# Kernel tuning notes

Measured on AMD Instinct MI355X. Metric: run time of the kernel, lower is better.

## Reference

```python
import jax, jax.numpy as jnp
from jax import lax
import numpy as np

ALPHA = 0.5   # init alpha
TEMP = 0.1    # init temp (used in nt_xent_loss)
TEMP2 = 0.05  # hardcoded temperature inside nt_xent_loss2
EPS = 1e-12

N, D, C = 4096, 128, 20


def setup_inputs() -> dict:
    key = jax.random.key(0)
    k1, k2, k3 = jax.random.split(key, 3)
    cls_feats = jax.random.normal(k1, (N, D), dtype=jnp.float32)
    predicts = jax.random.normal(k2, (N, C), dtype=jnp.float32)
    targets = jax.random.randint(k3, (N,), 0, C)
    return {"cls_feats": cls_feats, "predicts": predicts, "targets": targets}


def _forward(cls_feats, predicts, targets):
    n = cls_feats.shape[0]
    # F.normalize(dim=-1): x / max(||x||, eps)
    norms = jnp.maximum(jnp.linalg.norm(cls_feats, axis=-1, keepdims=True), EPS)
    feats = cls_feats / norms

    # --- cross entropy (mean reduction) ---
    logp_cls = jax.nn.log_softmax(predicts, axis=-1)
    ce_loss = -jnp.mean(jnp.take_along_axis(logp_cls, targets[:, None], axis=1))

    same = (targets[:, None] == targets[None, :]).astype(feats.dtype)  # [N,N]
    diff = 1.0 - same

    # --- nt_xent_loss (supervised contrastive, mask excludes diagonal) ---
    mask = same * (1.0 - jnp.eye(n, dtype=feats.dtype))
    logits = jnp.matmul(feats, feats.T) / TEMP
    logits = logits - lax.stop_gradient(jnp.max(logits, axis=1, keepdims=True))
    exp_logits = jnp.exp(logits) * mask
    log_prob = logits - jnp.log(jnp.sum(exp_logits, axis=1, keepdims=True) + EPS)
    mask_sum = jnp.sum(mask, axis=1)
    mask_sum = jnp.where(mask_sum == 0, 1.0, mask_sum)
    cl_loss = -jnp.mean(jnp.sum(mask * log_prob, axis=1) / mask_sum)

    # --- nt_xent_loss2, vectorized ---
    # In the torch loop, negtive_indices always equals arange(N) (same-label
    # indices include i; union with diff-label indices covers everything).
    # Row j of the per-i masked matrix is: zeros if label[j]==label[i], else
    # D2[j,:]*diff[j,:] (independent of i). A zero row contributes N to the
    # stabilized exp-sum; masked zeros contribute exp(-rowmax) entries, which
    # the single precomputation below reproduces exactly.
    D2 = jnp.matmul(feats, feats.T) / TEMP2
    B = D2 * diff                                  # [N,N]
    r = jnp.sum(jnp.exp(B - jnp.max(B, axis=1, keepdims=True)), axis=1)  # [N]
    c = jnp.sum(diff, axis=1)                      # diff-label count per row
    n_same = jnp.sum(same, axis=1)
    S = jnp.matmul(diff, r) + n_same * n           # sum over all rows j of exp-sums
    S = jnp.where(c > 0, S, 0.0)                   # 'continue' when no diff label
    negsum = jnp.matmul(diff, c)                   # ((1-same_rows)*diff).sum() per i
    all_zero = jnp.all(negsum == 0)
    x = jnp.where(all_zero, S, S / jnp.where(negsum == 0, 1.0, negsum))
    logp = -jnp.log(x + EPS)                       # per-row scalar
    ms2 = jnp.sum(same, axis=1)                    # >= 1 (includes self)
    pos_logits = jnp.sum(same * logp[:, None], axis=1) / ms2
    triple_loss = -jnp.mean(pos_logits)

    return (1.0 - ALPHA) * ce_loss + ALPHA * cl_loss + 0.5 * ALPHA * triple_loss


def reference(cls_feats, predicts, targets):
    return _forward(cls_feats, predicts, targets)
```

## Files before the change

kernel.cpp:

```cpp
#include <hip/hip_runtime.h>
#include <hip/hip_bf16.h>

#define NN 4096
#define DD 128
#define CC 20
#define NSPLIT 8
#define COLS_PER_SPLIT (NN / NSPLIT)
#define ROWS_PER_BLOCK 16
#define NSTRIP (NN / ROWS_PER_BLOCK)
#define BSTRIDE 152

typedef __attribute__((ext_vector_type(8))) short short8;
typedef __attribute__((ext_vector_type(4))) float floatx4;

__global__ void k_normalize(const float* __restrict__ x, __hip_bfloat16* __restrict__ out) {
    int wave = threadIdx.x >> 6;
    int lane = threadIdx.x & 63;
    int row  = blockIdx.x * 4 + wave;
    const float* xr = x + (size_t)row * DD;
    float2 v = *(const float2*)(xr + lane * 2);
    float ss = v.x * v.x + v.y * v.y;
    #pragma unroll
    for (int m = 1; m <= 32; m <<= 1) ss += __shfl_xor(ss, m);
    float nrm = sqrtf(ss);
    float inv = 1.0f / fmaxf(nrm, 1e-12f);
    __hip_bfloat162 h;
    h.x = __float2bfloat16(v.x * inv);
    h.y = __float2bfloat16(v.y * inv);
    *(__hip_bfloat162*)(out + (size_t)row * DD + lane * 2) = h;
}

__launch_bounds__(64, 2)
__global__ void k_gram_stats(const __hip_bfloat16* __restrict__ feats,
                             const int* __restrict__ tgt,
                             float* __restrict__ E1p, float* __restrict__ T1p,
                             float* __restrict__ C1p, float* __restrict__ m2p,
                             float* __restrict__ E2p) {
    __shared__ __align__(16) unsigned short Bt[64 * BSTRIDE];
    int lane  = threadIdx.x;
    int strip = blockIdx.x & (NSTRIP - 1);
    int split = blockIdx.x >> 8;
    int rbase  = strip * ROWS_PER_BLOCK;
    int cbase0 = split * COLS_PER_SPLIT;
    int lr = lane & 15, lk = lane >> 4;

    short8 afrag[4];
    const __hip_bfloat16* arow = feats + (size_t)(rbase + lr) * DD;
    #pragma unroll
    for (int kc = 0; kc < 4; ++kc)
        afrag[kc] = *(const short8*)(arow + kc * 32 + lk * 8);

    int rl[4], gr[4];
    #pragma unroll
    for (int q = 0; q < 4; ++q) { gr[q] = rbase + lk * 4 + q; rl[q] = tgt[gr[q]]; }

    float E1[4] = {0,0,0,0}, T1[4] = {0,0,0,0}, C1[4] = {0,0,0,0};
    float m2[4] = {0,0,0,0}, E2[4] = {0,0,0,0};

    for (int t = 0; t < COLS_PER_SPLIT / 64; ++t) {
        int cbase = cbase0 + t * 64;
        #pragma unroll
        for (int i = 0; i < 16; ++i) {
            int idx = lane + i * 64;
            int row = idx >> 4, ch = idx & 15;
            *(floatx4*)(&Bt[row * BSTRIDE + ch * 8]) =
                *(const floatx4*)(feats + (size_t)(cbase + row) * DD + ch * 8);
        }
        __syncthreads();
        #pragma unroll
        for (int sc = 0; sc < 4; ++sc) {
            floatx4 acc = {0.0f, 0.0f, 0.0f, 0.0f};
            #pragma unroll
            for (int kc = 0; kc < 4; ++kc) {
                short8 b = *(const short8*)(&Bt[(sc * 16 + lr) * BSTRIDE + kc * 32 + lk * 8]);
                acc = __builtin_amdgcn_mfma_f32_16x16x32_bf16(afrag[kc], b, acc, 0, 0, 0);
            }
            int gc   = cbase + sc * 16 + lr;
            int clab = tgt[gc];
            #pragma unroll
            for (int q = 0; q < 4; ++q) {
                float g = acc[q];
                bool same = (rl[q] == clab);
                bool v1   = same && (gr[q] != gc);
                float l1 = g * 10.0f;
                float l2 = g * 20.0f;
                float l1v = v1 ? l1 : -__builtin_inff();
                E1[q] += __expf(l1v - 10.0f);
                T1[q] += v1 ? l1 : 0.0f;
                C1[q] += v1 ? 1.0f : 0.0f;
                float l2v = same ? -__builtin_inff() : l2;
                float nm  = fmaxf(m2[q], l2v);
                E2[q] = E2[q] * __expf(m2[q] - nm) + __expf(l2v - nm);
                m2[q] = nm;
            }
        }
        __syncthreads();
    }

    #pragma unroll
    for (int q = 0; q < 4; ++q) {
        float e1 = E1[q], t1 = T1[q], c1 = C1[q], mm = m2[q], e2 = E2[q];
        #pragma unroll
        for (int m = 1; m <= 8; m <<= 1) {
            e1 += __shfl_xor(e1, m);
            t1 += __shfl_xor(t1, m);
            c1 += __shfl_xor(c1, m);
            float om = __shfl_xor(mm, m), oe = __shfl_xor(e2, m);
            float nm = fmaxf(mm, om);
            e2 = e2 * __expf(mm - nm) + oe * __expf(om - nm);
            mm = nm;
        }
        if (lr == 0) {
            int r = gr[q];
            E1p[split * NN + r] = e1;
            T1p[split * NN + r] = t1;
            C1p[split * NN + r] = c1;
            m2p[split * NN + r] = mm;
            E2p[split * NN + r] = e2;
        }
    }
}

#define FT 1024
__global__ void k_finalize(const float* __restrict__ predicts, const int* __restrict__ tgt,
                           const float* __restrict__ E1p, const float* __restrict__ T1p,
                           const float* __restrict__ C1p, const float* __restrict__ m2p,
                           const float* __restrict__ E2p, float* __restrict__ out) {
    __shared__ int   hist[CC];
    __shared__ float Rt[CC];
    __shared__ float sred[FT];
    __shared__ float s_cl;
    int t = threadIdx.x;
    if (t < CC) { hist[t] = 0; Rt[t] = 0.0f; }
    __syncthreads();
    for (int r = t; r < NN; r += FT) atomicAdd(&hist[tgt[r]], 1);
    __syncthreads();

    float clsum = 0.0f, cesum = 0.0f;
    for (int r = t; r < NN; r += FT) {
        int tg = tgt[r];
        float e1 = 0.0f, t1 = 0.0f, c1 = 0.0f, mg = 0.0f;
        float mv[NSPLIT], ev[NSPLIT];
        #pragma unroll
        for (int s = 0; s < NSPLIT; ++s) {
            e1 += E1p[s * NN + r];
            t1 += T1p[s * NN + r];
            c1 += C1p[s * NN + r];
            mv[s] = m2p[s * NN + r];
            ev[s] = E2p[s * NN + r];
            mg = fmaxf(mg, mv[s]);
        }
        float e2 = 0.0f;
        #pragma unroll
        for (int s = 0; s < NSPLIT; ++s) e2 += ev[s] * __expf(mv[s] - mg);

        if (c1 > 0.0f) clsum += (t1 - c1 * (10.0f + logf(e1))) / c1;

        float rj = (float)hist[tg] * __expf(-mg) + e2;
        atomicAdd(&Rt[tg], rj);

        const float* p = predicts + (size_t)r * CC;
        float mx = p[0];
        #pragma unroll
        for (int j = 1; j < CC; ++j) mx = fmaxf(mx, p[j]);
        float se = 0.0f;
        #pragma unroll
        for (int j = 0; j < CC; ++j) se += __expf(p[j] - mx);
        cesum += mx + logf(se) - p[tg];
    }

    sred[t] = clsum; __syncthreads();
    for (int off = FT / 2; off > 0; off >>= 1) {
        if (t < off) sred[t] += sred[t + off];
        __syncthreads();
    }
    if (t == 0) s_cl = sred[0];
    __syncthreads();
    sred[t] = cesum; __syncthreads();
    for (int off = FT / 2; off > 0; off >>= 1) {
        if (t < off) sred[t] += sred[t + off];
        __syncthreads();
    }
    if (t == 0) {
        float ce = sred[0] / (float)NN;
        float cl = -s_cl / (float)NN;
        float Rtot = 0.0f;
        long long Ctot = 0;
        for (int k = 0; k < CC; ++k) {
            Rtot += Rt[k];
            Ctot += (long long)hist[k] * (NN - hist[k]);
        }
        bool all_zero = true;
        for (int k = 0; k < CC; ++k)
            if (hist[k] > 0 && (Ctot - (long long)hist[k] * (NN - hist[k])) != 0) all_zero = false;
        float trip = 0.0f;
        for (int k = 0; k < CC; ++k) {
            if (hist[k] == 0) continue;
            long long c = NN - hist[k];
            float S = (c > 0) ? (Rtot - Rt[k] + (float)hist[k] * (float)NN) : 0.0f;
            long long ns = Ctot - (long long)hist[k] * (NN - hist[k]);
            float x = all_zero ? S : S / (float)(ns == 0 ? 1 : ns);
            trip += (float)hist[k] * logf(x + 1e-12f);
        }
        float triple = trip / (float)NN;
        out[0] = 0.5f * ce + 0.5f * cl + 0.25f * triple;
    }
}

extern "C" void kernel_launch(void* const* d_in, const int* in_sizes, int n_in,
                              void* d_out, int out_size, void* d_ws, size_t ws_size,
                              hipStream_t stream) {
    const float* cls  = (const float*)d_in[0];
    const float* pred = (const float*)d_in[1];
    const int*   tgt  = (const int*)d_in[2];
    float* out = (float*)d_out;
    char* ws = (char*)d_ws;

    __hip_bfloat16* feats = (__hip_bfloat16*)ws;
    float* E1p = (float*)(ws + 1048576);
    float* T1p = E1p + (size_t)NSPLIT * NN;
    float* C1p = T1p + (size_t)NSPLIT * NN;
    float* m2p = C1p + (size_t)NSPLIT * NN;
    float* E2p = m2p + (size_t)NSPLIT * NN;

    hipLaunchKernelGGL(k_normalize, dim3(NN / 4), dim3(256), 0, stream, cls, feats);
    hipLaunchKernelGGL(k_gram_stats, dim3(NSTRIP * NSPLIT), dim3(64), 0, stream,
                       feats, tgt, E1p, T1p, C1p, m2p, E2p);
    hipLaunchKernelGGL(k_finalize, dim3(1), dim3(FT), 0, stream,
                       pred, tgt, E1p, T1p, C1p, m2p, E2p, out);
}
```

Before: 101.9 us.

## Fixed-shift exp stats, atomic accumulation, CE moved into prep, 4-wave gram blocks

```diff
diff --git a/kernel.cpp b/kernel.cpp
--- a/kernel.cpp
+++ b/kernel.cpp
@@ -4,44 +4,61 @@
 #define NN 4096
 #define DD 128
 #define CC 20
-#define NSPLIT 8
-#define COLS_PER_SPLIT (NN / NSPLIT)
-#define ROWS_PER_BLOCK 16
+#define NSPLIT 16
+#define CPS (NN / NSPLIT)
+#define ROWS_PER_WAVE 16
+#define ROWS_PER_BLOCK 64
 #define NSTRIP (NN / ROWS_PER_BLOCK)
 #define BSTRIDE 152
 
 typedef __attribute__((ext_vector_type(8))) short short8;
 typedef __attribute__((ext_vector_type(4))) float floatx4;
 
-__global__ void k_normalize(const float* __restrict__ x, __hip_bfloat16* __restrict__ out) {
-    int wave = threadIdx.x >> 6;
-    int lane = threadIdx.x & 63;
-    int row  = blockIdx.x * 4 + wave;
+__global__ void k_prep(const float* __restrict__ x, const float* __restrict__ pred,
+                       const int* __restrict__ tgt,
+                       __hip_bfloat16* __restrict__ feats,
+                       float* __restrict__ statsz,
+                       float* __restrict__ ce_part) {
+    __shared__ float ce_w[4];
+    int wave = threadIdx.x >> 6, lane = threadIdx.x & 63;
+    int row = blockIdx.x * 4 + wave;
+    if (threadIdx.x < 16) statsz[blockIdx.x * 16 + threadIdx.x] = 0.0f;
     const float* xr = x + (size_t)row * DD;
     float2 v = *(const float2*)(xr + lane * 2);
     float ss = v.x * v.x + v.y * v.y;
     #pragma unroll
     for (int m = 1; m <= 32; m <<= 1) ss += __shfl_xor(ss, m);
-    float nrm = sqrtf(ss);
-    float inv = 1.0f / fmaxf(nrm, 1e-12f);
+    float inv = 1.0f / fmaxf(sqrtf(ss), 1e-12f);
     __hip_bfloat162 h;
     h.x = __float2bfloat16(v.x * inv);
     h.y = __float2bfloat16(v.y * inv);
-    *(__hip_bfloat162*)(out + (size_t)row * DD + lane * 2) = h;
-}
-
-__launch_bounds__(64, 2)
+    *(__hip_bfloat162*)(feats + (size_t)row * DD + lane * 2) = h;
+    float p = (lane < CC) ? pred[(size_t)row * CC + lane] : -__builtin_inff();
+    float mx = p;
+    #pragma unroll
+    for (int m = 1; m <= 32; m <<= 1) mx = fmaxf(mx, __shfl_xor(mx, m));
+    float e = (lane < CC) ? __expf(p - mx) : 0.0f;
+    #pragma unroll
+    for (int m = 1; m <= 32; m <<= 1) e += __shfl_xor(e, m);
+    float ptg = __shfl(p, tgt[row]);
+    if (lane == 0) ce_w[wave] = mx + logf(e) - ptg;
+    __syncthreads();
+    if (threadIdx.x == 0)
+        ce_part[blockIdx.x] = ce_w[0] + ce_w[1] + ce_w[2] + ce_w[3];
+}
+
+__launch_bounds__(256, 4)
 __global__ void k_gram_stats(const __hip_bfloat16* __restrict__ feats,
                              const int* __restrict__ tgt,
-                             float* __restrict__ E1p, float* __restrict__ T1p,
-                             float* __restrict__ C1p, float* __restrict__ m2p,
-                             float* __restrict__ E2p) {
+                             float* __restrict__ E1g, float* __restrict__ T1g,
+                             float* __restrict__ E2g, float* __restrict__ M2g) {
     __shared__ __align__(16) unsigned short Bt[64 * BSTRIDE];
-    int lane  = threadIdx.x;
+    int lane  = threadIdx.x & 63;
+    int wave  = threadIdx.x >> 6;
     int strip = blockIdx.x & (NSTRIP - 1);
-    int split = blockIdx.x >> 8;
-    int rbase  = strip * ROWS_PER_BLOCK;
-    int cbase0 = split * COLS_PER_SPLIT;
+    int split = blockIdx.x >> 6;
+    int rbase  = strip * ROWS_PER_BLOCK + wave * ROWS_PER_WAVE;
+    int cbase0 = split * CPS;
     int lr = lane & 15, lk = lane >> 4;
 
     short8 afrag[4];
@@ -54,14 +71,13 @@
     #pragma unroll
     for (int q = 0; q < 4; ++q) { gr[q] = rbase + lk * 4 + q; rl[q] = tgt[gr[q]]; }
 
-    float E1[4] = {0,0,0,0}, T1[4] = {0,0,0,0}, C1[4] = {0,0,0,0};
-    float m2[4] = {0,0,0,0}, E2[4] = {0,0,0,0};
-
-    for (int t = 0; t < COLS_PER_SPLIT / 64; ++t) {
+    float E1[4] = {0,0,0,0}, T1[4] = {0,0,0,0}, E2[4] = {0,0,0,0}, m2[4] = {0,0,0,0};
+
+    for (int t = 0; t < CPS / 64; ++t) {
         int cbase = cbase0 + t * 64;
         #pragma unroll
-        for (int i = 0; i < 16; ++i) {
-            int idx = lane + i * 64;
+        for (int i = 0; i < 4; ++i) {
+            int idx = threadIdx.x + i * 256;
             int row = idx >> 4, ch = idx & 15;
             *(floatx4*)(&Bt[row * BSTRIDE + ch * 8]) =
                 *(const floatx4*)(feats + (size_t)(cbase + row) * DD + ch * 8);
@@ -79,19 +95,15 @@
             int clab = tgt[gc];
             #pragma unroll
             for (int q = 0; q < 4; ++q) {
-                float g = acc[q];
+                float g  = acc[q];
+                float l1 = g * 10.0f;
+                float tv = __expf(l1 - 10.0f);
                 bool same = (rl[q] == clab);
                 bool v1   = same && (gr[q] != gc);
-                float l1 = g * 10.0f;
-                float l2 = g * 20.0f;
-                float l1v = v1 ? l1 : -__builtin_inff();
-                E1[q] += __expf(l1v - 10.0f);
+                E1[q] += v1 ? tv : 0.0f;
                 T1[q] += v1 ? l1 : 0.0f;
-                C1[q] += v1 ? 1.0f : 0.0f;
-                float l2v = same ? -__builtin_inff() : l2;
-                float nm  = fmaxf(m2[q], l2v);
-                E2[q] = E2[q] * __expf(m2[q] - nm) + __expf(l2v - nm);
-                m2[q] = nm;
+                E2[q] += same ? 0.0f : tv * tv;
+                m2[q] = fmaxf(m2[q], same ? 0.0f : l1 + l1);
             }
         }
         __syncthreads();
@@ -99,36 +111,32 @@
 
     #pragma unroll
     for (int q = 0; q < 4; ++q) {
-        float e1 = E1[q], t1 = T1[q], c1 = C1[q], mm = m2[q], e2 = E2[q];
+        float e1 = E1[q], t1 = T1[q], e2 = E2[q], mm = m2[q];
         #pragma unroll
         for (int m = 1; m <= 8; m <<= 1) {
             e1 += __shfl_xor(e1, m);
             t1 += __shfl_xor(t1, m);
-            c1 += __shfl_xor(c1, m);
-            float om = __shfl_xor(mm, m), oe = __shfl_xor(e2, m);
-            float nm = fmaxf(mm, om);
-            e2 = e2 * __expf(mm - nm) + oe * __expf(om - nm);
-            mm = nm;
+            e2 += __shfl_xor(e2, m);
+            mm = fmaxf(mm, __shfl_xor(mm, m));
         }
         if (lr == 0) {
             int r = gr[q];
-            E1p[split * NN + r] = e1;
-            T1p[split * NN + r] = t1;
-            C1p[split * NN + r] = c1;
-            m2p[split * NN + r] = mm;
-            E2p[split * NN + r] = e2;
-        }
-    }
-}
-
-#define FT 1024
-__global__ void k_finalize(const float* __restrict__ predicts, const int* __restrict__ tgt,
-                           const float* __restrict__ E1p, const float* __restrict__ T1p,
-                           const float* __restrict__ C1p, const float* __restrict__ m2p,
-                           const float* __restrict__ E2p, float* __restrict__ out) {
+            atomicAdd(&E1g[r], e1);
+            atomicAdd(&T1g[r], t1);
+            atomicAdd(&E2g[r], e2);
+            atomicMax((int*)&M2g[r], __float_as_int(mm));
+        }
+    }
+}
+
+#define FT 256
+__global__ void k_finalize(const int* __restrict__ tgt,
+                           const float* __restrict__ E1g, const float* __restrict__ T1g,
+                           const float* __restrict__ E2g, const float* __restrict__ M2g,
+                           const float* __restrict__ ce_part, float* __restrict__ out) {
     __shared__ int   hist[CC];
     __shared__ float Rt[CC];
-    __shared__ float sred[FT];
+    __shared__ float red[FT];
     __shared__ float s_cl;
     int t = threadIdx.x;
     if (t < CC) { hist[t] = 0; Rt[t] = 0.0f; }
@@ -136,53 +144,33 @@
     for (int r = t; r < NN; r += FT) atomicAdd(&hist[tgt[r]], 1);
     __syncthreads();
 
-    float clsum = 0.0f, cesum = 0.0f;
+    float clsum = 0.0f;
     for (int r = t; r < NN; r += FT) {
         int tg = tgt[r];
-        float e1 = 0.0f, t1 = 0.0f, c1 = 0.0f, mg = 0.0f;
-        float mv[NSPLIT], ev[NSPLIT];
-        #pragma unroll
-        for (int s = 0; s < NSPLIT; ++s) {
-            e1 += E1p[s * NN + r];
-            t1 += T1p[s * NN + r];
-            c1 += C1p[s * NN + r];
-            mv[s] = m2p[s * NN + r];
-            ev[s] = E2p[s * NN + r];
-            mg = fmaxf(mg, mv[s]);
-        }
-        float e2 = 0.0f;
-        #pragma unroll
-        for (int s = 0; s < NSPLIT; ++s) e2 += ev[s] * __expf(mv[s] - mg);
-
+        int h  = hist[tg];
+        float c1 = (float)(h - 1);
+        float e1 = E1g[r], t1 = T1g[r], e2 = E2g[r], m = M2g[r];
         if (c1 > 0.0f) clsum += (t1 - c1 * (10.0f + logf(e1))) / c1;
-
-        float rj = (float)hist[tg] * __expf(-mg) + e2;
+        float rj = (float)h * __expf(-m) + e2 * __expf(20.0f - m);
         atomicAdd(&Rt[tg], rj);
-
-        const float* p = predicts + (size_t)r * CC;
-        float mx = p[0];
-        #pragma unroll
-        for (int j = 1; j < CC; ++j) mx = fmaxf(mx, p[j]);
-        float se = 0.0f;
-        #pragma unroll
-        for (int j = 0; j < CC; ++j) se += __expf(p[j] - mx);
-        cesum += mx + logf(se) - p[tg];
-    }
-
-    sred[t] = clsum; __syncthreads();
-    for (int off = FT / 2; off > 0; off >>= 1) {
-        if (t < off) sred[t] += sred[t + off];
-        __syncthreads();
-    }
-    if (t == 0) s_cl = sred[0];
-    __syncthreads();
-    sred[t] = cesum; __syncthreads();
-    for (int off = FT / 2; off > 0; off >>= 1) {
-        if (t < off) sred[t] += sred[t + off];
+    }
+    float cesum = 0.0f;
+    for (int i = t; i < 1024; i += FT) cesum += ce_part[i];
+
+    red[t] = clsum; __syncthreads();
+    for (int off = FT / 2; off; off >>= 1) {
+        if (t < off) red[t] += red[t + off];
+        __syncthreads();
+    }
+    if (t == 0) s_cl = red[0];
+    __syncthreads();
+    red[t] = cesum; __syncthreads();
+    for (int off = FT / 2; off; off >>= 1) {
+        if (t < off) red[t] += red[t + off];
         __syncthreads();
     }
     if (t == 0) {
-        float ce = sred[0] / (float)NN;
+        float ce = red[0] / (float)NN;
         float cl = -s_cl / (float)NN;
         float Rtot = 0.0f;
         long long Ctot = 0;
@@ -217,15 +205,17 @@
     char* ws = (char*)d_ws;
 
     __hip_bfloat16* feats = (__hip_bfloat16*)ws;
-    float* E1p = (float*)(ws + 1048576);
-    float* T1p = E1p + (size_t)NSPLIT * NN;
-    float* C1p = T1p + (size_t)NSPLIT * NN;
-    float* m2p = C1p + (size_t)NSPLIT * NN;
-    float* E2p = m2p + (size_t)NSPLIT * NN;
-
-    hipLaunchKernelGGL(k_normalize, dim3(NN / 4), dim3(256), 0, stream, cls, feats);
-    hipLaunchKernelGGL(k_gram_stats, dim3(NSTRIP * NSPLIT), dim3(64), 0, stream,
-                       feats, tgt, E1p, T1p, C1p, m2p, E2p);
+    float* stats = (float*)(ws + 1048576);
+    float* E1g = stats;
+    float* T1g = stats + NN;
+    float* E2g = stats + 2 * NN;
+    float* M2g = stats + 3 * NN;
+    float* ce_part = stats + 4 * NN;
+
+    hipLaunchKernelGGL(k_prep, dim3(NN / 4), dim3(256), 0, stream,
+                       cls, pred, tgt, feats, stats, ce_part);
+    hipLaunchKernelGGL(k_gram_stats, dim3(NSTRIP * NSPLIT), dim3(256), 0, stream,
+                       feats, tgt, E1g, T1g, E2g, M2g);
     hipLaunchKernelGGL(k_finalize, dim3(1), dim3(FT), 0, stream,
-                       pred, tgt, E1p, T1p, C1p, m2p, E2p, out);
-}
+                       tgt, E1g, T1g, E2g, M2g, ce_part, out);
+}
```

Measured after the change: 94.60 us. 7.1% less time.
